# Kernel optimization log

Measured on AMD Instinct MI355X. Metric: run time of the kernel, lower is better.

Reference implementation:

```python
import jax, jax.numpy as jnp
import numpy as np

WIN = 11
SIGMA = 1.5
C1 = 0.01 ** 2
C2 = 0.03 ** 2


def _gauss1d():
    coords = jnp.arange(WIN, dtype=jnp.float32) - WIN // 2
    g = jnp.exp(-(coords ** 2) / (2.0 * SIGMA ** 2))
    return g / g.sum()


def _blur(x, g):
    C = x.shape[1]
    pad = WIN // 2
    dn = ('NCHW', 'OIHW', 'NCHW')
    kh = jnp.tile(g.reshape(1, 1, WIN, 1), (C, 1, 1, 1))
    kw = jnp.tile(g.reshape(1, 1, 1, WIN), (C, 1, 1, 1))
    x = jax.lax.conv_general_dilated(x, kh, (1, 1), ((pad, pad), (0, 0)),
                                     dimension_numbers=dn, feature_group_count=C)
    x = jax.lax.conv_general_dilated(x, kw, (1, 1), ((0, 0), (pad, pad)),
                                     dimension_numbers=dn, feature_group_count=C)
    return x


def _ssim_loss(pred, target, loss_weight=1.0):
    g = _gauss1d()
    mu1 = _blur(pred, g)
    mu2 = _blur(target, g)
    mu1_sq = mu1 * mu1
    mu2_sq = mu2 * mu2
    mu1_mu2 = mu1 * mu2
    sigma1_sq = _blur(pred * pred, g) - mu1_sq
    sigma2_sq = _blur(target * target, g) - mu2_sq
    sigma12 = _blur(pred * target, g) - mu1_mu2
    ssim_map = ((2.0 * mu1_mu2 + C1) * (2.0 * sigma12 + C2)) / \
               ((mu1_sq + mu2_sq + C1) * (sigma1_sq + sigma2_sq + C2))
    # size_average=True -> scalar mean; reduction='mean' on a scalar is identity
    return loss_weight * (1.0 - ssim_map.mean())


def setup_inputs() -> dict:
    key = jax.random.key(0)
    k1, k2 = jax.random.split(key)
    shape = (16, 3, 512, 512)
    pred = jax.random.uniform(k1, shape, dtype=jnp.float32)
    target = jax.random.uniform(k2, shape, dtype=jnp.float32)
    return {"pred": pred, "target": target}


def reference(pred, target):
    return _ssim_loss(pred, target, loss_weight=1.0)
```

## Files before the change

### kernel.cpp

```cpp
#include <hip/hip_runtime.h>

#define IMG 512
#define TW 32
#define TH 32
#define NG 12
#define VS 52
#define N_TOT (16 * 3 * 512 * 512)
#define NBLK (256 * 48)
#define NSLOT 1024

__device__ __constant__ const float Gw[11] = {
    0.00102838f, 0.00759876f, 0.03600077f, 0.10936086f, 0.21300537f,
    0.26601173f, 0.21300537f, 0.10936086f, 0.03600077f, 0.00759876f,
    0.00102838f};

__global__ __launch_bounds__(256) void ssim_main(const float* __restrict__ pred,
                                                 const float* __restrict__ tgt,
                                                 float* __restrict__ ws,
                                                 int parts_mode) {
    __shared__ __align__(16) float v[4][TH * VS];
    __shared__ float red[4];

    const int tid = threadIdx.x;
    const int tile = blockIdx.x;
    const int plane = blockIdx.y;
    const int tx = (tile & 15) * TW;
    const int ty = (tile >> 4) * TH;
    const float* pbase = pred + (size_t)plane * (IMG * IMG);
    const float* tbase = tgt + (size_t)plane * (IMG * IMG);

    if (tid < NG * 16) {
        const int g4 = tid % NG;
        const int rp = tid / NG;
        const int r0 = rp * 2;
        const int col = tx - 8 + (g4 << 2);
        const bool xin = (unsigned)col < (unsigned)IMG;
        const int ybase = ty + r0 - 5;

        float a0[4][4], a1[4][4];
#pragma unroll
        for (int q = 0; q < 4; ++q)
#pragma unroll
            for (int j = 0; j < 4; ++j) { a0[q][j] = 0.f; a1[q][j] = 0.f; }

#pragma unroll
        for (int k = 0; k < 12; ++k) {
            const int y = ybase + k;
            float4 P = make_float4(0.f, 0.f, 0.f, 0.f);
            float4 T = make_float4(0.f, 0.f, 0.f, 0.f);
            if (xin && (unsigned)y < (unsigned)IMG) {
                const int gidx = y * IMG + col;
                P = *(const float4*)(pbase + gidx);
                T = *(const float4*)(tbase + gidx);
            }
            const float p[4] = {P.x, P.y, P.z, P.w};
            const float t[4] = {T.x, T.y, T.z, T.w};
#pragma unroll
            for (int j = 0; j < 4; ++j) {
                const float ss = fmaf(p[j], p[j], t[j] * t[j]);
                const float pt = p[j] * t[j];
                if (k < 11) {
                    const float w = Gw[k];
                    a0[0][j] = fmaf(w, p[j], a0[0][j]);
                    a0[1][j] = fmaf(w, t[j], a0[1][j]);
                    a0[2][j] = fmaf(w, ss, a0[2][j]);
                    a0[3][j] = fmaf(w, pt, a0[3][j]);
                }
                if (k > 0) {
                    const float w = Gw[k - 1];
                    a1[0][j] = fmaf(w, p[j], a1[0][j]);
                    a1[1][j] = fmaf(w, t[j], a1[1][j]);
                    a1[2][j] = fmaf(w, ss, a1[2][j]);
                    a1[3][j] = fmaf(w, pt, a1[3][j]);
                }
            }
        }
        const int o = r0 * VS + (g4 << 2);
#pragma unroll
        for (int q = 0; q < 4; ++q) {
            *(float4*)(&v[q][o]) = make_float4(a0[q][0], a0[q][1], a0[q][2], a0[q][3]);
            *(float4*)(&v[q][o + VS]) = make_float4(a1[q][0], a1[q][1], a1[q][2], a1[q][3]);
        }
    }
    __syncthreads();

    float lsum = 0.f;
    {
        const int oy = tid >> 3;
        const int ox = (tid & 7) << 2;
        const int o = oy * VS + ox;

        float out[4][4];
#pragma unroll
        for (int q = 0; q < 4; ++q) {
            float win[20];
#pragma unroll
            for (int b = 0; b < 5; ++b) {
                const float4 W = *(const float4*)(&v[q][o + (b << 2)]);
                win[4 * b + 0] = W.x;
                win[4 * b + 1] = W.y;
                win[4 * b + 2] = W.z;
                win[4 * b + 3] = W.w;
            }
#pragma unroll
            for (int j = 0; j < 4; ++j) {
                float acc = 0.f;
#pragma unroll
                for (int k = 0; k < 11; ++k)
                    acc = fmaf(Gw[k], win[3 + j + k], acc);
                out[q][j] = acc;
            }
        }

        const float C1 = 0.0001f;
        const float C2 = 0.0009f;
#pragma unroll
        for (int j = 0; j < 4; ++j) {
            const float mu1 = out[0][j], mu2 = out[1][j];
            const float mu1s = mu1 * mu1;
            const float mu2s = mu2 * mu2;
            const float mu12 = mu1 * mu2;
            const float A = mu1s + mu2s;
            const float s12 = out[3][j] - mu12;
            const float sden = out[2][j] - A;
            const float num = fmaf(2.f, mu12, C1) * fmaf(2.f, s12, C2);
            const float den = (A + C1) * (sden + C2);
            lsum += num / den;
        }
    }

#pragma unroll
    for (int off = 32; off > 0; off >>= 1) lsum += __shfl_down(lsum, off, 64);
    if ((tid & 63) == 0) red[tid >> 6] = lsum;
    __syncthreads();
    if (tid == 0) {
        const float bs = red[0] + red[1] + red[2] + red[3];
        const int bid = blockIdx.y * gridDim.x + blockIdx.x;
        if (parts_mode) {
            ws[bid] = bs;
        } else {
            atomicAdd(&ws[bid & (NSLOT - 1)], bs);
        }
    }
}

__global__ __launch_bounds__(256) void ssim_final(const float* __restrict__ ws,
                                                  float* __restrict__ out, int count) {
    __shared__ float red[4];
    const int tid = threadIdx.x;
    float s = 0.f;
    for (int i = tid; i < count; i += 256) s += ws[i];
#pragma unroll
    for (int off = 32; off > 0; off >>= 1) s += __shfl_down(s, off, 64);
    if ((tid & 63) == 0) red[tid >> 6] = s;
    __syncthreads();
    if (tid == 0) {
        const float tot = red[0] + red[1] + red[2] + red[3];
        out[0] = 1.0f - tot * (1.0f / (float)N_TOT);
    }
}

extern "C" void kernel_launch(void* const* d_in, const int* in_sizes, int n_in,
                              void* d_out, int out_size, void* d_ws, size_t ws_size,
                              hipStream_t stream) {
    const float* pred = (const float*)d_in[0];
    const float* tgt = (const float*)d_in[1];
    float* out = (float*)d_out;
    float* ws = (float*)d_ws;

    const int parts_mode = (ws_size >= (size_t)NBLK * sizeof(float)) ? 1 : 0;
    if (!parts_mode) {
        hipMemsetAsync(ws, 0, NSLOT * sizeof(float), stream);
    }
    dim3 grid(256, 48);
    ssim_main<<<grid, 256, 0, stream>>>(pred, tgt, ws, parts_mode);
    ssim_final<<<1, 256, 0, stream>>>(ws, out, parts_mode ? NBLK : NSLOT);
}
```

Baseline: 177.1 us.

## Interleave blur channels as float4 in LDS, shrink block to 192, fast interior path

Stores the four vertical-blur quantities interleaved as one float4 per column in shared memory, so the horizontal pass reads 14 float4 values per output group instead of 20 floats per channel. The block shrinks to 192 threads so every thread does vertical work; the 256 horizontal outputs are then covered in a strided loop, leaving some threads with two iterations. Interior tiles skip bounds checks on global loads, and the final reduction reads the workspace as float4. The costs are an uneven second pass and a different LDS bank-access pattern.

```diff
diff --git a/kernel.cpp b/kernel.cpp
--- a/kernel.cpp
+++ b/kernel.cpp
@@ -4,7 +4,7 @@
 #define TW 32
 #define TH 32
 #define NG 12
-#define VS 52
+#define S4 49
 #define N_TOT (16 * 3 * 512 * 512)
 #define NBLK (256 * 48)
 #define NSLOT 1024
@@ -14,27 +14,53 @@
     0.26601173f, 0.21300537f, 0.10936086f, 0.03600077f, 0.00759876f,
     0.00102838f};
 
-__global__ __launch_bounds__(256) void ssim_main(const float* __restrict__ pred,
+__device__ __forceinline__ void vtaps(const float4 P, const float4 T, const int k,
+                                      float a0[4][4], float a1[4][4]) {
+    const float p[4] = {P.x, P.y, P.z, P.w};
+    const float t[4] = {T.x, T.y, T.z, T.w};
+#pragma unroll
+    for (int j = 0; j < 4; ++j) {
+        const float ss = fmaf(p[j], p[j], t[j] * t[j]);
+        const float pt = p[j] * t[j];
+        if (k < 11) {
+            const float w = Gw[k];
+            a0[0][j] = fmaf(w, p[j], a0[0][j]);
+            a0[1][j] = fmaf(w, t[j], a0[1][j]);
+            a0[2][j] = fmaf(w, ss, a0[2][j]);
+            a0[3][j] = fmaf(w, pt, a0[3][j]);
+        }
+        if (k > 0) {
+            const float w = Gw[k - 1];
+            a1[0][j] = fmaf(w, p[j], a1[0][j]);
+            a1[1][j] = fmaf(w, t[j], a1[1][j]);
+            a1[2][j] = fmaf(w, ss, a1[2][j]);
+            a1[3][j] = fmaf(w, pt, a1[3][j]);
+        }
+    }
+}
+
+__global__ __launch_bounds__(192) void ssim_main(const float* __restrict__ pred,
                                                  const float* __restrict__ tgt,
                                                  float* __restrict__ ws,
                                                  int parts_mode) {
-    __shared__ __align__(16) float v[4][TH * VS];
-    __shared__ float red[4];
+    __shared__ __align__(16) float4 v4[TH * S4];
+    __shared__ float red[3];
 
     const int tid = threadIdx.x;
     const int tile = blockIdx.x;
     const int plane = blockIdx.y;
-    const int tx = (tile & 15) * TW;
-    const int ty = (tile >> 4) * TH;
+    const int tile_x = tile & 15;
+    const int tile_y = tile >> 4;
+    const int tx = tile_x * TW;
+    const int ty = tile_y * TH;
     const float* pbase = pred + (size_t)plane * (IMG * IMG);
     const float* tbase = tgt + (size_t)plane * (IMG * IMG);
 
-    if (tid < NG * 16) {
+    {
         const int g4 = tid % NG;
         const int rp = tid / NG;
         const int r0 = rp * 2;
         const int col = tx - 8 + (g4 << 2);
-        const bool xin = (unsigned)col < (unsigned)IMG;
         const int ybase = ty + r0 - 5;
 
         float a0[4][4], a1[4][4];
@@ -43,86 +69,71 @@
 #pragma unroll
             for (int j = 0; j < 4; ++j) { a0[q][j] = 0.f; a1[q][j] = 0.f; }
 
+        const bool interior = (tile_x >= 1) && (tile_x <= 14) && (tile_y >= 1) && (tile_y <= 14);
+        if (interior) {
+            const float* pp = pbase + (ybase * IMG + col);
+            const float* tp = tbase + (ybase * IMG + col);
 #pragma unroll
-        for (int k = 0; k < 12; ++k) {
-            const int y = ybase + k;
-            float4 P = make_float4(0.f, 0.f, 0.f, 0.f);
-            float4 T = make_float4(0.f, 0.f, 0.f, 0.f);
-            if (xin && (unsigned)y < (unsigned)IMG) {
-                const int gidx = y * IMG + col;
-                P = *(const float4*)(pbase + gidx);
-                T = *(const float4*)(tbase + gidx);
+            for (int k = 0; k < 12; ++k) {
+                const float4 P = *(const float4*)(pp + k * IMG);
+                const float4 T = *(const float4*)(tp + k * IMG);
+                vtaps(P, T, k, a0, a1);
             }
-            const float p[4] = {P.x, P.y, P.z, P.w};
-            const float t[4] = {T.x, T.y, T.z, T.w};
+        } else {
+            const bool xin = (unsigned)col < (unsigned)IMG;
 #pragma unroll
-            for (int j = 0; j < 4; ++j) {
-                const float ss = fmaf(p[j], p[j], t[j] * t[j]);
-                const float pt = p[j] * t[j];
-                if (k < 11) {
-                    const float w = Gw[k];
-                    a0[0][j] = fmaf(w, p[j], a0[0][j]);
-                    a0[1][j] = fmaf(w, t[j], a0[1][j]);
-                    a0[2][j] = fmaf(w, ss, a0[2][j]);
-                    a0[3][j] = fmaf(w, pt, a0[3][j]);
+            for (int k = 0; k < 12; ++k) {
+                const int y = ybase + k;
+                float4 P = make_float4(0.f, 0.f, 0.f, 0.f);
+                float4 T = make_float4(0.f, 0.f, 0.f, 0.f);
+                if (xin && (unsigned)y < (unsigned)IMG) {
+                    const int gidx = y * IMG + col;
+                    P = *(const float4*)(pbase + gidx);
+                    T = *(const float4*)(tbase + gidx);
                 }
-                if (k > 0) {
-                    const float w = Gw[k - 1];
-                    a1[0][j] = fmaf(w, p[j], a1[0][j]);
-                    a1[1][j] = fmaf(w, t[j], a1[1][j]);
-                    a1[2][j] = fmaf(w, ss, a1[2][j]);
-                    a1[3][j] = fmaf(w, pt, a1[3][j]);
-                }
+                vtaps(P, T, k, a0, a1);
             }
         }
-        const int o = r0 * VS + (g4 << 2);
+
+        float4* w0 = &v4[r0 * S4 + (g4 << 2)];
+        float4* w1 = w0 + S4;
 #pragma unroll
-        for (int q = 0; q < 4; ++q) {
-            *(float4*)(&v[q][o]) = make_float4(a0[q][0], a0[q][1], a0[q][2], a0[q][3]);
-            *(float4*)(&v[q][o + VS]) = make_float4(a1[q][0], a1[q][1], a1[q][2], a1[q][3]);
+        for (int j = 0; j < 4; ++j) {
+            w0[j] = make_float4(a0[0][j], a0[1][j], a0[2][j], a0[3][j]);
+            w1[j] = make_float4(a1[0][j], a1[1][j], a1[2][j], a1[3][j]);
         }
     }
     __syncthreads();
 
     float lsum = 0.f;
-    {
-        const int oy = tid >> 3;
-        const int ox = (tid & 7) << 2;
-        const int o = oy * VS + ox;
-
-        float out[4][4];
+    for (int s = tid; s < 256; s += 192) {
+        const int oy = s >> 3;
+        const int ox = (s & 7) << 2;
+        const float4* row = &v4[oy * S4 + ox + 3];
+        float4 win[14];
 #pragma unroll
-        for (int q = 0; q < 4; ++q) {
-            float win[20];
-#pragma unroll
-            for (int b = 0; b < 5; ++b) {
-                const float4 W = *(const float4*)(&v[q][o + (b << 2)]);
-                win[4 * b + 0] = W.x;
-                win[4 * b + 1] = W.y;
-                win[4 * b + 2] = W.z;
-                win[4 * b + 3] = W.w;
-            }
-#pragma unroll
-            for (int j = 0; j < 4; ++j) {
-                float acc = 0.f;
-#pragma unroll
-                for (int k = 0; k < 11; ++k)
-                    acc = fmaf(Gw[k], win[3 + j + k], acc);
-                out[q][j] = acc;
-            }
-        }
+        for (int i = 0; i < 14; ++i) win[i] = row[i];
 
         const float C1 = 0.0001f;
         const float C2 = 0.0009f;
 #pragma unroll
         for (int j = 0; j < 4; ++j) {
-            const float mu1 = out[0][j], mu2 = out[1][j];
-            const float mu1s = mu1 * mu1;
-            const float mu2s = mu2 * mu2;
-            const float mu12 = mu1 * mu2;
+            float m1 = 0.f, m2 = 0.f, bss = 0.f, bpt = 0.f;
+#pragma unroll
+            for (int k = 0; k < 11; ++k) {
+                const float4 W = win[j + k];
+                const float w = Gw[k];
+                m1 = fmaf(w, W.x, m1);
+                m2 = fmaf(w, W.y, m2);
+                bss = fmaf(w, W.z, bss);
+                bpt = fmaf(w, W.w, bpt);
+            }
+            const float mu1s = m1 * m1;
+            const float mu2s = m2 * m2;
+            const float mu12 = m1 * m2;
             const float A = mu1s + mu2s;
-            const float s12 = out[3][j] - mu12;
-            const float sden = out[2][j] - A;
+            const float s12 = bpt - mu12;
+            const float sden = bss - A;
             const float num = fmaf(2.f, mu12, C1) * fmaf(2.f, s12, C2);
             const float den = (A + C1) * (sden + C2);
             lsum += num / den;
@@ -134,7 +145,7 @@
     if ((tid & 63) == 0) red[tid >> 6] = lsum;
     __syncthreads();
     if (tid == 0) {
-        const float bs = red[0] + red[1] + red[2] + red[3];
+        const float bs = red[0] + red[1] + red[2];
         const int bid = blockIdx.y * gridDim.x + blockIdx.x;
         if (parts_mode) {
             ws[bid] = bs;
@@ -144,18 +155,21 @@
     }
 }
 
-__global__ __launch_bounds__(256) void ssim_final(const float* __restrict__ ws,
-                                                  float* __restrict__ out, int count) {
+__global__ __launch_bounds__(256) void ssim_final(const float4* __restrict__ ws4,
+                                                  float* __restrict__ out, int count4) {
     __shared__ float red[4];
     const int tid = threadIdx.x;
     float s = 0.f;
-    for (int i = tid; i < count; i += 256) s += ws[i];
+    for (int i = tid; i < count4; i += 256) {
+        const float4 w = ws4[i];
+        s += (w.x + w.y) + (w.z + w.w);
+    }
 #pragma unroll
     for (int off = 32; off > 0; off >>= 1) s += __shfl_down(s, off, 64);
     if ((tid & 63) == 0) red[tid >> 6] = s;
     __syncthreads();
     if (tid == 0) {
-        const float tot = red[0] + red[1] + red[2] + red[3];
+        const float tot = (red[0] + red[1]) + (red[2] + red[3]);
         out[0] = 1.0f - tot * (1.0f / (float)N_TOT);
     }
 }
@@ -173,6 +187,7 @@
         hipMemsetAsync(ws, 0, NSLOT * sizeof(float), stream);
     }
     dim3 grid(256, 48);
-    ssim_main<<<grid, 256, 0, stream>>>(pred, tgt, ws, parts_mode);
-    ssim_final<<<1, 256, 0, stream>>>(ws, out, parts_mode ? NBLK : NSLOT);
+    ssim_main<<<grid, 192, 0, stream>>>(pred, tgt, ws, parts_mode);
+    ssim_final<<<1, 256, 0, stream>>>((const float4*)ws, out,
+                                      (parts_mode ? NBLK : NSLOT) / 4);
 }
```

Result: slower. 268.3 us (+51.5%).
